# Performance work log

Hardware: AMD Instinct MI355X
Metric: run time of the kernel (lower is better)

## Reference

```python
import jax, jax.numpy as jnp
import numpy as np

NUM_HEADS = 16
HEAD_DIM = 80
DIM = NUM_HEADS * HEAD_DIM
SEQ = 2048
SCALE = HEAD_DIM ** -0.5


def rotate_half(x):
    x1, x2 = jnp.split(x, 2, axis=-1)
    return jnp.concatenate((-x2, x1), axis=-1)


def setup_inputs() -> dict:
    key = jax.random.key(0)
    ks = jax.random.split(key, 8)
    hidden_states = jax.random.normal(ks[0], (SEQ, DIM), dtype=jnp.float32)
    cu_seqlens = jnp.array([0, SEQ], dtype=jnp.int32)  # unused by the math
    # rotary embeddings for head_dim
    inv_freq = 1.0 / (10000.0 ** (jnp.arange(0, HEAD_DIM // 2, dtype=jnp.float32) / (HEAD_DIM // 2)))
    freqs = jnp.outer(jnp.arange(SEQ, dtype=jnp.float32), inv_freq)  # [S, hd/2]
    emb = jnp.concatenate((freqs, freqs), axis=-1)  # [S, hd]
    cos = jnp.cos(emb)
    sin = jnp.sin(emb)
    w_qkv = jax.random.normal(ks[1], (3 * DIM, DIM), dtype=jnp.float32) * (DIM ** -0.5)
    b_qkv = jax.random.normal(ks[2], (3 * DIM,), dtype=jnp.float32) * 0.02
    w_proj = jax.random.normal(ks[3], (DIM, DIM), dtype=jnp.float32) * (DIM ** -0.5)
    b_proj = jax.random.normal(ks[4], (DIM,), dtype=jnp.float32) * 0.02
    return {"hidden_states": hidden_states, "cu_seqlens": cu_seqlens, "cos": cos,
            "sin": sin, "w_qkv": w_qkv, "b_qkv": b_qkv, "w_proj": w_proj, "b_proj": b_proj}


def reference(hidden_states, cu_seqlens, cos, sin, w_qkv, b_qkv, w_proj, b_proj):
    S = hidden_states.shape[0]
    qkv = hidden_states @ w_qkv.T + b_qkv  # [S, 3*D]
    qkv = qkv.reshape(S, 3, NUM_HEADS, HEAD_DIM)
    q, k, v = qkv[:, 0], qkv[:, 1], qkv[:, 2]  # each [S, H, hd]
    c = cos[:, None, :]  # [S, 1, hd]
    s = sin[:, None, :]
    q = q * c + rotate_half(q) * s
    k = k * c + rotate_half(k) * s
    # SDPA, non-causal: [H, S, S]
    scores = jnp.einsum('shd,thd->hst', q, k) * SCALE
    attn = jax.nn.softmax(scores, axis=-1)
    out = jnp.einsum('hst,thd->shd', attn, v).reshape(S, DIM)
    return out @ w_proj.T + b_proj
```

## Files before the change

### kernel.cpp

```cpp
#include <hip/hip_runtime.h>


#define SEQLEN   2048
#define DIMM     1280
#define NHEADS   16
#define HD       80
#define QKV_N    3840
#define NSPLIT   4
#define KVSPAN   (SEQLEN / NSPLIT)
#define QSCALE_LOG2E 0.16130083587064776f

#define KSTRIDE  88
#define VFSTRIDE 24

#define EXP2F(x) __builtin_amdgcn_exp2f(x)

#define GLD16(gptr, lptr)                                                      \
    __builtin_amdgcn_global_load_lds(                                          \
        (const __attribute__((address_space(1))) void*)(gptr),                 \
        (__attribute__((address_space(3))) void*)(lptr), 16, 0, 0)

typedef float f32x4 __attribute__((ext_vector_type(4)));
typedef _Float16 half8 __attribute__((ext_vector_type(8)));
typedef _Float16 half4 __attribute__((ext_vector_type(4)));
typedef _Float16 half2v __attribute__((ext_vector_type(2)));

static __device__ __forceinline__ f32x4 mfma_16x16x32(half8 a, half8 b, f32x4 c) {
    return __builtin_amdgcn_mfma_f32_16x16x32_f16(a, b, c, 0, 0, 0);
}
static __device__ __forceinline__ f32x4 mfma_16x16x16(half4 a, half4 b, f32x4 c) {
    return __builtin_amdgcn_mfma_f32_16x16x16f16(a, b, c, 0, 0, 0);
}
static __device__ __forceinline__ half4 lo4(half8 v) {
    return __builtin_shufflevector(v, v, 0, 1, 2, 3);
}
static __device__ __forceinline__ half4 hi4(half8 v) {
    return __builtin_shufflevector(v, v, 4, 5, 6, 7);
}

__global__ __launch_bounds__(256)
void cast_all(const float* __restrict__ hs, const float* __restrict__ wq,
              const float* __restrict__ wp, _Float16* __restrict__ dhs,
              _Float16* __restrict__ dwq, _Float16* __restrict__ dwp) {
    const int n1 = SEQLEN * DIMM / 4, n2 = QKV_N * DIMM / 4, n3 = DIMM * DIMM / 4;
    int i = blockIdx.x * 256 + threadIdx.x;
    const float4* src; half4* dst; int j;
    if (i < n1)           { src = (const float4*)hs; dst = (half4*)dhs; j = i; }
    else if (i < n1 + n2) { src = (const float4*)wq; dst = (half4*)dwq; j = i - n1; }
    else if (i < n1 + n2 + n3) { src = (const float4*)wp; dst = (half4*)dwp; j = i - n1 - n2; }
    else return;
    const float4 v = src[j];
    half4 h;
    h.x = (_Float16)v.x; h.y = (_Float16)v.y;
    h.z = (_Float16)v.z; h.w = (_Float16)v.w;
    dst[j] = h;
}

template<bool OUT_F16>
__global__ __launch_bounds__(512, 4)
void gemm_bt128(const _Float16* __restrict__ A, const _Float16* __restrict__ B,
                const float* __restrict__ bias, void* __restrict__ Cout,
                int M, int N, int K) {
    __shared__ __align__(16) _Float16 As[2][128 * 32];
    __shared__ __align__(16) _Float16 Bs[2][128 * 32];
    const int tid  = threadIdx.x;
    const int lane = tid & 63;
    const int wave = tid >> 6;
    const int l15  = lane & 15;
    const int quad = lane >> 4;
    const int wm   = wave & 3;
    const int wn   = wave >> 2;
    const long bm = blockIdx.x, bn = blockIdx.y;

    const _Float16* Ag = A + bm * 128 * (long)K;
    const _Float16* Bg = B + bn * 128 * (long)K;

    const int srow = lane >> 2;
    const int scol = (lane & 3) * 8;
    f32x4 acc[2][4] = {};

    for (int k0 = 0; k0 < K; k0 += 64) {
        __syncthreads();
#pragma unroll
        for (int p = 0; p < 2; p++) {
            const int kp = k0 + p * 32;
            const long r = 16 * wave + srow;
            GLD16(Ag + r * K + kp + scol, &As[p][512 * wave + lane * 8]);
            GLD16(Bg + r * K + kp + scol, &Bs[p][512 * wave + lane * 8]);
        }
        __syncthreads();
#pragma unroll
        for (int p = 0; p < 2; p++) {
            half8 af[2], bf[4];
#pragma unroll
            for (int t = 0; t < 2; t++)
                af[t] = *(const half8*)&As[p][(wm * 32 + t * 16 + l15) * 32 + quad * 8];
#pragma unroll
            for (int t = 0; t < 4; t++)
                bf[t] = *(const half8*)&Bs[p][(wn * 64 + t * 16 + l15) * 32 + quad * 8];
#pragma unroll
            for (int mt = 0; mt < 2; mt++)
#pragma unroll
                for (int nt = 0; nt < 4; nt++)
                    acc[mt][nt] = mfma_16x16x32(af[mt], bf[nt], acc[mt][nt]);
        }
    }

    float bv[4];
#pragma unroll
    for (int nt = 0; nt < 4; nt++)
        bv[nt] = bias[bn * 128 + wn * 64 + nt * 16 + l15];

#pragma unroll
    for (int mt = 0; mt < 2; mt++) {
#pragma unroll
        for (int r = 0; r < 4; r++) {
            const long row = bm * 128 + wm * 32 + mt * 16 + quad * 4 + r;
#pragma unroll
            for (int nt = 0; nt < 4; nt++) {
                const long col = bn * 128 + wn * 64 + nt * 16 + l15;
                const float v = acc[mt][nt][r] + bv[nt];
                if (OUT_F16) ((_Float16*)Cout)[row * (long)N + col] = (_Float16)v;
                else         ((float*)Cout)[row * (long)N + col] = v;
            }
        }
    }
}

template<bool OUT_F16>
__global__ __launch_bounds__(256, 2)
void gemm_bt64(const _Float16* __restrict__ A, const _Float16* __restrict__ B,
               const float* __restrict__ bias, void* __restrict__ Cout,
               int M, int N, int K) {
    __shared__ __align__(16) _Float16 As[2][64 * 32];
    __shared__ __align__(16) _Float16 Bs[2][128 * 32];
    const int tid  = threadIdx.x;
    const int lane = tid & 63;
    const int wave = tid >> 6;
    const int l15  = lane & 15;
    const int quad = lane >> 4;
    const int wm   = wave & 1;
    const int wn   = wave >> 1;
    const long bm = blockIdx.x, bn = blockIdx.y;

    const _Float16* Ag = A + bm * 64 * (long)K;
    const _Float16* Bg = B + bn * 128 * (long)K;

    const int srow = lane >> 2;
    const int scol = (lane & 3) * 8;
    f32x4 acc[2][4] = {};

    for (int k0 = 0; k0 < K; k0 += 64) {
        __syncthreads();
#pragma unroll
        for (int p = 0; p < 2; p++) {
            const int kp = k0 + p * 32;
            const long arow = 16 * wave + srow;
            GLD16(Ag + arow * K + kp + scol, &As[p][512 * wave + lane * 8]);
#pragma unroll
            for (int cc = 0; cc < 2; cc++) {
                const int c = wave + cc * 4;
                const long brow = 16 * c + srow;
                GLD16(Bg + brow * K + kp + scol, &Bs[p][512 * c + lane * 8]);
            }
        }
        __syncthreads();
#pragma unroll
        for (int p = 0; p < 2; p++) {
            half8 af[2], bf[4];
#pragma unroll
            for (int t = 0; t < 2; t++)
                af[t] = *(const half8*)&As[p][(wm * 32 + t * 16 + l15) * 32 + quad * 8];
#pragma unroll
            for (int t = 0; t < 4; t++)
                bf[t] = *(const half8*)&Bs[p][(wn * 64 + t * 16 + l15) * 32 + quad * 8];
#pragma unroll
            for (int mt = 0; mt < 2; mt++)
#pragma unroll
                for (int nt = 0; nt < 4; nt++)
                    acc[mt][nt] = mfma_16x16x32(af[mt], bf[nt], acc[mt][nt]);
        }
    }

    float bv[4];
#pragma unroll
    for (int nt = 0; nt < 4; nt++)
        bv[nt] = bias[bn * 128 + wn * 64 + nt * 16 + l15];

#pragma unroll
    for (int mt = 0; mt < 2; mt++) {
#pragma unroll
        for (int r = 0; r < 4; r++) {
            const long row = bm * 64 + wm * 32 + mt * 16 + quad * 4 + r;
#pragma unroll
            for (int nt = 0; nt < 4; nt++) {
                const long col = bn * 128 + wn * 64 + nt * 16 + l15;
                const float v = acc[mt][nt][r] + bv[nt];
                if (OUT_F16) ((_Float16*)Cout)[row * (long)N + col] = (_Float16)v;
                else         ((float*)Cout)[row * (long)N + col] = v;
            }
        }
    }
}

__global__ __launch_bounds__(256)
void rope_repack_t(const _Float16* __restrict__ qkv,
                   const float* __restrict__ cosb,
                   const float* __restrict__ sinb,
                   _Float16* __restrict__ Qh,
                   _Float16* __restrict__ Kh,
                   _Float16* __restrict__ Vt) {
    const int s0 = blockIdx.x * 64;
    const int h  = blockIdx.y;
    __shared__ __align__(16) _Float16 Ts[64 * 88];
    const int tid = threadIdx.x;

    for (int i = tid; i < 640; i += 256) {
        const int r = i / 10, c = (i - r * 10) * 8;
        *(half8*)&Ts[r * 88 + c] =
            *(const half8*)&qkv[(long)(s0 + r) * QKV_N + 2 * DIMM + h * HD + c];
    }

    for (int i = tid; i < 320; i += 256) {
        const int r = i / 5, d = (i - r * 5) * 8;
        const _Float16* row = qkv + (long)(s0 + r) * QKV_N + h * HD;
        const half8 q0 = *(const half8*)&row[d];
        const half8 q1 = *(const half8*)&row[d + 40];
        const half8 k0 = *(const half8*)&row[DIMM + d];
        const half8 k1 = *(const half8*)&row[DIMM + d + 40];
        const float4 cA = *(const float4*)&cosb[(s0 + r) * HD + d];
        const float4 cB = *(const float4*)&cosb[(s0 + r) * HD + d + 4];
        const float4 sA = *(const float4*)&sinb[(s0 + r) * HD + d];
        const float4 sB = *(const float4*)&sinb[(s0 + r) * HD + d + 4];
        half8 qo0, qo1, ko0, ko1;
#pragma unroll
        for (int j = 0; j < 8; j++) {
            const float cj = (j < 4) ? cA[j] : cB[j - 4];
            const float sj = (j < 4) ? sA[j] : sB[j - 4];
            qo0[j] = (_Float16)(((float)q0[j] * cj - (float)q1[j] * sj) * QSCALE_LOG2E);
            qo1[j] = (_Float16)(((float)q1[j] * cj + (float)q0[j] * sj) * QSCALE_LOG2E);
            ko0[j] = (_Float16)((float)k0[j] * cj - (float)k1[j] * sj);
            ko1[j] = (_Float16)((float)k1[j] * cj + (float)k0[j] * sj);
        }
        const long o = ((long)h * SEQLEN + s0 + r) * HD;
        *(half8*)&Qh[o + d]      = qo0;
        *(half8*)&Qh[o + d + 40] = qo1;
        *(half8*)&Kh[o + d]      = ko0;
        *(half8*)&Kh[o + d + 40] = ko1;
    }
    __syncthreads();
    for (int i = tid; i < 640; i += 256) {
        const int d = i >> 3, sc = (i & 7) * 8;
        half8 v;
#pragma unroll
        for (int j = 0; j < 8; j++) v[j] = Ts[(sc + j) * 88 + d];
        *(half8*)&Vt[((long)h * HD + d) * SEQLEN + s0 + sc] = v;
    }
}

__global__ __launch_bounds__(512, 4)
void attn_kernel(const _Float16* __restrict__ Qh, const _Float16* __restrict__ Kh,
                 const _Float16* __restrict__ Vt,
                 _Float16* __restrict__ Ohat0, _Float16* __restrict__ Ohat1,
                 float* __restrict__ Lpart) {
    const int s0 = blockIdx.x * 256;
    const int h  = blockIdx.y;
    const int z  = blockIdx.z;
    __shared__ __align__(16) _Float16 Ks[64 * KSTRIDE];
    __shared__ __align__(16) _Float16 VF[5 * 64 * VFSTRIDE];

    const int tid  = threadIdx.x;
    const int lane = tid & 63;
    const int wave = tid >> 6;
    const int l15  = lane & 15;
    const int quad = lane >> 4;

    const int zBeg = z * KVSPAN, zEnd = zBeg + KVSPAN;

    const _Float16* Qg0 = Qh + ((long)h * SEQLEN + s0 + wave * 32 + l15) * HD;
    const _Float16* Qg1 = Qg0 + 16 * (long)HD;
    const half8 qA0 = *(const half8*)&Qg0[quad * 8];
    const half8 qA1 = *(const half8*)&Qg0[32 + quad * 8];
    const half4 qA2 = *(const half4*)&Qg0[64 + quad * 4];
    const half8 qB0 = *(const half8*)&Qg1[quad * 8];
    const half8 qB1 = *(const half8*)&Qg1[32 + quad * 8];
    const half4 qB2 = *(const half4*)&Qg1[64 + quad * 4];

    int offA, dsA, offB, dsB0, dsB1 = 0, offC = 0, dsC0 = 0, dsC1 = 0;
    {
        const int rA = tid / 10, cA = (tid - rA * 10) * 8;
        offA = rA * HD + cA;
        dsA  = rA * KSTRIDE + cA;
        if (tid < 128) {
            const int cB = tid + 512;
            const int rB = cB / 10, ccB = (cB - rB * 10) * 8;
            offB = rB * HD + ccB;
            dsB0 = rB * KSTRIDE + ccB;
        } else {
            const int v = tid - 128, d = v >> 3, c8 = (v & 7) * 8;
            offB = d * SEQLEN + c8;
            const int nt = d >> 4, ld = d & 15, ct = c8 >> 4, qb = (c8 & 15) >> 2;
            dsB0 = (nt * 64 + qb * 16 + ld) * VFSTRIDE + ct * 4;
            dsB1 = (nt * 64 + (qb + 1) * 16 + ld) * VFSTRIDE + ct * 4;
        }
        if (tid < 256) {
            const int v = tid + 384, d = v >> 3, c8 = (v & 7) * 8;
            offC = d * SEQLEN + c8;
            const int nt = d >> 4, ld = d & 15, ct = c8 >> 4, qb = (c8 & 15) >> 2;
            dsC0 = (nt * 64 + qb * 16 + ld) * VFSTRIDE + ct * 4;
            dsC1 = (nt * 64 + (qb + 1) * 16 + ld) * VFSTRIDE + ct * 4;
        }
    }
    const _Float16* KzBase = Kh + ((long)h * SEQLEN + zBeg) * HD;
    const _Float16* VzBase = Vt + (long)h * HD * SEQLEN + zBeg;

    f32x4 oaccA[5] = {}, oaccB[5] = {};
    float laA0 = 0.f, laA1 = 0.f, laB0 = 0.f, laB1 = 0.f;
    const half2v ones2 = {(_Float16)1.f, (_Float16)1.f};

    for (int t0 = zBeg; t0 < zEnd; t0 += 64) {
        const _Float16* KzT = KzBase + (long)(t0 - zBeg) * HD;
        const _Float16* VzT = VzBase + (t0 - zBeg);
        const half8 a = *(const half8*)(KzT + offA);
        half8 b;
        if (tid < 128) b = *(const half8*)(KzT + offB);
        else           b = *(const half8*)(VzT + offB);
        half8 cv = {};
        if (tid < 256) cv = *(const half8*)(VzT + offC);

        __syncthreads();
        *(half8*)&Ks[dsA] = a;
        if (tid < 128) { *(half8*)&Ks[dsB0] = b; }
        else {
            *(half4*)&VF[dsB0] = lo4(b);
            *(half4*)&VF[dsB1] = hi4(b);
        }
        if (tid < 256) {
            *(half4*)&VF[dsC0] = lo4(cv);
            *(half4*)&VF[dsC1] = hi4(cv);
        }
        __syncthreads();

        f32x4 saA[4] = {}, saB[4] = {};
        __builtin_amdgcn_s_setprio(1);
#pragma unroll
        for (int ct = 0; ct < 4; ct++) {
            const int kb = (ct * 16 + l15) * KSTRIDE;
            const half8 kf0 = *(const half8*)&Ks[kb + quad * 8];
            const half8 kf1 = *(const half8*)&Ks[kb + 32 + quad * 8];
            const half4 kf2 = *(const half4*)&Ks[kb + 64 + quad * 4];
            saA[ct] = mfma_16x16x32(kf0, qA0, saA[ct]);
            saB[ct] = mfma_16x16x32(kf0, qB0, saB[ct]);
            saA[ct] = mfma_16x16x32(kf1, qA1, saA[ct]);
            saB[ct] = mfma_16x16x32(kf1, qB1, saB[ct]);
            saA[ct] = mfma_16x16x16(kf2, qA2, saA[ct]);
            saB[ct] = mfma_16x16x16(kf2, qB2, saB[ct]);
        }
        __builtin_amdgcn_s_setprio(0);

        half4 pbA[4], pbB[4];
#pragma unroll
        for (int ct = 0; ct < 4; ct++) {
            {
                const float e0 = EXP2F(saA[ct][0]);
                const float e1 = EXP2F(saA[ct][1]);
                const float e2 = EXP2F(saA[ct][2]);
                const float e3 = EXP2F(saA[ct][3]);
                const half2v p01 = __builtin_bit_cast(half2v, __builtin_amdgcn_cvt_pkrtz(e0, e1));
                const half2v p23 = __builtin_bit_cast(half2v, __builtin_amdgcn_cvt_pkrtz(e2, e3));
                laA0 = __builtin_amdgcn_fdot2(p01, ones2, laA0, false);
                laA1 = __builtin_amdgcn_fdot2(p23, ones2, laA1, false);
                pbA[ct] = __builtin_shufflevector(p01, p23, 0, 1, 2, 3);
            }
            {
                const float e0 = EXP2F(saB[ct][0]);
                const float e1 = EXP2F(saB[ct][1]);
                const float e2 = EXP2F(saB[ct][2]);
                const float e3 = EXP2F(saB[ct][3]);
                const half2v p01 = __builtin_bit_cast(half2v, __builtin_amdgcn_cvt_pkrtz(e0, e1));
                const half2v p23 = __builtin_bit_cast(half2v, __builtin_amdgcn_cvt_pkrtz(e2, e3));
                laB0 = __builtin_amdgcn_fdot2(p01, ones2, laB0, false);
                laB1 = __builtin_amdgcn_fdot2(p23, ones2, laB1, false);
                pbB[ct] = __builtin_shufflevector(p01, p23, 0, 1, 2, 3);
            }
        }

        __builtin_amdgcn_s_setprio(1);
#pragma unroll
        for (int nt = 0; nt < 5; nt++) {
            const half8 va = *(const half8*)&VF[(nt * 64 + lane) * VFSTRIDE];
            const half8 vb = *(const half8*)&VF[(nt * 64 + lane) * VFSTRIDE + 8];
            oaccA[nt] = mfma_16x16x16(lo4(va), pbA[0], oaccA[nt]);
            oaccB[nt] = mfma_16x16x16(lo4(va), pbB[0], oaccB[nt]);
            oaccA[nt] = mfma_16x16x16(hi4(va), pbA[1], oaccA[nt]);
            oaccB[nt] = mfma_16x16x16(hi4(va), pbB[1], oaccB[nt]);
            oaccA[nt] = mfma_16x16x16(lo4(vb), pbA[2], oaccA[nt]);
            oaccB[nt] = mfma_16x16x16(lo4(vb), pbB[2], oaccB[nt]);
            oaccA[nt] = mfma_16x16x16(hi4(vb), pbA[3], oaccA[nt]);
            oaccB[nt] = mfma_16x16x16(hi4(vb), pbB[3], oaccB[nt]);
        }
        __builtin_amdgcn_s_setprio(0);
    }

    float lA = laA0 + laA1, lB = laB0 + laB1;
    lA += __shfl_xor(lA, 16); lA += __shfl_xor(lA, 32);
    lB += __shfl_xor(lB, 16); lB += __shfl_xor(lB, 32);
    const float invA = 1.0f / lA, invB = 1.0f / lB;

    _Float16* Oz = (z < 2) ? Ohat0 : Ohat1;
    const long obase = ((long)(z & 1) * NHEADS + h) * SEQLEN;
    const long lbase = ((long)z * NHEADS + h) * SEQLEN;
    const long rowA = s0 + wave * 32 + l15;
    const long rowB = rowA + 16;
#pragma unroll
    for (int nt = 0; nt < 5; nt++) {
        half4 oA, oB;
#pragma unroll
        for (int r = 0; r < 4; r++) {
            oA[r] = (_Float16)(oaccA[nt][r] * invA);
            oB[r] = (_Float16)(oaccB[nt][r] * invB);
        }
        *(half4*)&Oz[(obase + rowA) * HD + nt * 16 + quad * 4] = oA;
        *(half4*)&Oz[(obase + rowB) * HD + nt * 16 + quad * 4] = oB;
    }
    if (quad == 0) {
        Lpart[lbase + rowA] = lA;
        Lpart[lbase + rowB] = lB;
    }
}

__global__ __launch_bounds__(256)
void attn_combine(const _Float16* __restrict__ Ohat0,
                  const _Float16* __restrict__ Ohat1,
                  const float* __restrict__ Lp,
                  _Float16* __restrict__ attnb) {
    const int i = blockIdx.x * 256 + threadIdx.x;
    if (i >= SEQLEN * DIMM / 4) return;
    const int flat = i * 4;
    const int s = flat / DIMM;
    const int rem = flat - s * DIMM;
    const int h = rem / HD;
    const int d = rem - h * HD;
    float l[NSPLIT], lsum = 0.f;
#pragma unroll
    for (int zi = 0; zi < NSPLIT; zi++) {
        l[zi] = Lp[((long)zi * NHEADS + h) * SEQLEN + s];
        lsum += l[zi];
    }
    const float invl = 1.0f / lsum;
    float acc[4] = {0.f, 0.f, 0.f, 0.f};
#pragma unroll
    for (int zi = 0; zi < NSPLIT; zi++) {
        const _Float16* Oz = (zi < 2) ? Ohat0 : Ohat1;
        const long obase = ((long)(zi & 1) * NHEADS + h) * SEQLEN;
        const half4 o = *(const half4*)&Oz[(obase + s) * HD + d];
        const float w = l[zi] * invl;
#pragma unroll
        for (int j = 0; j < 4; j++) acc[j] += (float)o[j] * w;
    }
    half4 o;
#pragma unroll
    for (int j = 0; j < 4; j++) o[j] = (_Float16)acc[j];
    *(half4*)&attnb[(long)s * DIMM + rem] = o;
}

extern "C" void kernel_launch(void* const* d_in, const int* in_sizes, int n_in,
                              void* d_out, int out_size, void* d_ws, size_t ws_size,
                              hipStream_t stream) {
    const float* hs     = (const float*)d_in[0];
    const float* cosb   = (const float*)d_in[2];
    const float* sinb   = (const float*)d_in[3];
    const float* w_qkv  = (const float*)d_in[4];
    const float* b_qkv  = (const float*)d_in[5];
    const float* w_proj = (const float*)d_in[6];
    const float* b_proj = (const float*)d_in[7];
    float* out = (float*)d_out;

    _Float16* hsb    = (_Float16*)d_ws;
    _Float16* wqkvb  = hsb    + (long)SEQLEN * DIMM;
    _Float16* wprojb = wqkvb  + (long)QKV_N * DIMM;
    _Float16* qkv    = wprojb + (long)DIMM * DIMM;
    _Float16* Qh     = qkv    + (long)SEQLEN * QKV_N;
    _Float16* Kh     = Qh     + (long)NHEADS * SEQLEN * HD;
    _Float16* Vtb    = Kh     + (long)NHEADS * SEQLEN * HD;
    _Float16* attnb  = Vtb    + (long)NHEADS * HD * SEQLEN;

    _Float16* Ohat0  = (_Float16*)d_ws;
    float*    LpartB = (float*)(Ohat0 + (long)2 * NHEADS * SEQLEN * HD);
    _Float16* Ohat1  = qkv;

    {
        const int ntot = (SEQLEN * DIMM + QKV_N * DIMM + DIMM * DIMM) / 4;
        cast_all<<<(ntot + 255) / 256, 256, 0, stream>>>(
            hs, w_qkv, w_proj, hsb, wqkvb, wprojb);
    }

    gemm_bt128<true><<<dim3(SEQLEN / 128, QKV_N / 128), 512, 0, stream>>>(
        hsb, wqkvb, b_qkv, qkv, SEQLEN, QKV_N, DIMM);

    rope_repack_t<<<dim3(SEQLEN / 64, NHEADS), 256, 0, stream>>>(
        qkv, cosb, sinb, Qh, Kh, Vtb);

    attn_kernel<<<dim3(SEQLEN / 256, NHEADS, NSPLIT), 512, 0, stream>>>(
        Qh, Kh, Vtb, Ohat0, Ohat1, LpartB);

    attn_combine<<<(SEQLEN * DIMM / 4 + 255) / 256, 256, 0, stream>>>(
        Ohat0, Ohat1, LpartB, attnb);

    gemm_bt64<false><<<dim3(SEQLEN / 64, DIMM / 128), 256, 0, stream>>>(
        attnb, wprojb, b_proj, out, SEQLEN, DIMM, DIMM);
}
```

Measured before the change: 187.6 us.

## Double-buffer K/V tiles in attention LDS, widen combine vectors, raise gemm occupancy

The attention kernel now keeps two LDS buffers for its K and V tiles. It prefetches the next 64-key tile into the alternate buffer after the PV MFMAs, which removes one of the two barriers per iteration and lets global loads overlap with compute. The cost is doubled LDS use, about 44KB per block, which may limit occupancy at 4 blocks per CU. The combine kernel now processes 8 halves per thread instead of 4, since HD=80 is divisible by 8, and the projection GEMM's launch-bounds occupancy hint goes from 2 to 4.

```diff
diff --git a/kernel.cpp b/kernel.cpp
--- a/kernel.cpp
+++ b/kernel.cpp
@@ -12,6 +12,8 @@
 
 #define KSTRIDE  88
 #define VFSTRIDE 24
+#define VFOFF    (64 * KSTRIDE)
+#define BUFH     (64 * KSTRIDE + 5 * 64 * VFSTRIDE)
 
 #define EXP2F(x) __builtin_amdgcn_exp2f(x)
 
@@ -128,7 +130,7 @@
 }
 
 template<bool OUT_F16>
-__global__ __launch_bounds__(256, 2)
+__global__ __launch_bounds__(256, 4)
 void gemm_bt64(const _Float16* __restrict__ A, const _Float16* __restrict__ B,
                const float* __restrict__ bias, void* __restrict__ Cout,
                int M, int N, int K) {
@@ -266,8 +268,7 @@
     const int s0 = blockIdx.x * 256;
     const int h  = blockIdx.y;
     const int z  = blockIdx.z;
-    __shared__ __align__(16) _Float16 Ks[64 * KSTRIDE];
-    __shared__ __align__(16) _Float16 VF[5 * 64 * VFSTRIDE];
+    __shared__ __align__(16) _Float16 Sb[2 * BUFH];
 
     const int tid  = threadIdx.x;
     const int lane = tid & 63;
@@ -300,55 +301,55 @@
             const int v = tid - 128, d = v >> 3, c8 = (v & 7) * 8;
             offB = d * SEQLEN + c8;
             const int nt = d >> 4, ld = d & 15, ct = c8 >> 4, qb = (c8 & 15) >> 2;
-            dsB0 = (nt * 64 + qb * 16 + ld) * VFSTRIDE + ct * 4;
-            dsB1 = (nt * 64 + (qb + 1) * 16 + ld) * VFSTRIDE + ct * 4;
+            dsB0 = VFOFF + (nt * 64 + qb * 16 + ld) * VFSTRIDE + ct * 4;
+            dsB1 = VFOFF + (nt * 64 + (qb + 1) * 16 + ld) * VFSTRIDE + ct * 4;
         }
         if (tid < 256) {
             const int v = tid + 384, d = v >> 3, c8 = (v & 7) * 8;
             offC = d * SEQLEN + c8;
             const int nt = d >> 4, ld = d & 15, ct = c8 >> 4, qb = (c8 & 15) >> 2;
-            dsC0 = (nt * 64 + qb * 16 + ld) * VFSTRIDE + ct * 4;
-            dsC1 = (nt * 64 + (qb + 1) * 16 + ld) * VFSTRIDE + ct * 4;
+            dsC0 = VFOFF + (nt * 64 + qb * 16 + ld) * VFSTRIDE + ct * 4;
+            dsC1 = VFOFF + (nt * 64 + (qb + 1) * 16 + ld) * VFSTRIDE + ct * 4;
         }
     }
     const _Float16* KzBase = Kh + ((long)h * SEQLEN + zBeg) * HD;
     const _Float16* VzBase = Vt + (long)h * HD * SEQLEN + zBeg;
+
+    {
+        const half8 a = *(const half8*)(KzBase + offA);
+        half8 b;
+        if (tid < 128) b = *(const half8*)(KzBase + offB);
+        else           b = *(const half8*)(VzBase + offB);
+        half8 cv = {};
+        if (tid < 256) cv = *(const half8*)(VzBase + offC);
+        *(half8*)&Sb[dsA] = a;
+        if (tid < 128) { *(half8*)&Sb[dsB0] = b; }
+        else {
+            *(half4*)&Sb[dsB0] = lo4(b);
+            *(half4*)&Sb[dsB1] = hi4(b);
+        }
+        if (tid < 256) {
+            *(half4*)&Sb[dsC0] = lo4(cv);
+            *(half4*)&Sb[dsC1] = hi4(cv);
+        }
+    }
 
     f32x4 oaccA[5] = {}, oaccB[5] = {};
     float laA0 = 0.f, laA1 = 0.f, laB0 = 0.f, laB1 = 0.f;
     const half2v ones2 = {(_Float16)1.f, (_Float16)1.f};
+    int cb = 0;
 
     for (int t0 = zBeg; t0 < zEnd; t0 += 64) {
-        const _Float16* KzT = KzBase + (long)(t0 - zBeg) * HD;
-        const _Float16* VzT = VzBase + (t0 - zBeg);
-        const half8 a = *(const half8*)(KzT + offA);
-        half8 b;
-        if (tid < 128) b = *(const half8*)(KzT + offB);
-        else           b = *(const half8*)(VzT + offB);
-        half8 cv = {};
-        if (tid < 256) cv = *(const half8*)(VzT + offC);
-
-        __syncthreads();
-        *(half8*)&Ks[dsA] = a;
-        if (tid < 128) { *(half8*)&Ks[dsB0] = b; }
-        else {
-            *(half4*)&VF[dsB0] = lo4(b);
-            *(half4*)&VF[dsB1] = hi4(b);
-        }
-        if (tid < 256) {
-            *(half4*)&VF[dsC0] = lo4(cv);
-            *(half4*)&VF[dsC1] = hi4(cv);
-        }
         __syncthreads();
 
         f32x4 saA[4] = {}, saB[4] = {};
         __builtin_amdgcn_s_setprio(1);
 #pragma unroll
         for (int ct = 0; ct < 4; ct++) {
-            const int kb = (ct * 16 + l15) * KSTRIDE;
-            const half8 kf0 = *(const half8*)&Ks[kb + quad * 8];
-            const half8 kf1 = *(const half8*)&Ks[kb + 32 + quad * 8];
-            const half4 kf2 = *(const half4*)&Ks[kb + 64 + quad * 4];
+            const int kb = cb + (ct * 16 + l15) * KSTRIDE;
+            const half8 kf0 = *(const half8*)&Sb[kb + quad * 8];
+            const half8 kf1 = *(const half8*)&Sb[kb + 32 + quad * 8];
+            const half4 kf2 = *(const half4*)&Sb[kb + 64 + quad * 4];
             saA[ct] = mfma_16x16x32(kf0, qA0, saA[ct]);
             saB[ct] = mfma_16x16x32(kf0, qB0, saB[ct]);
             saA[ct] = mfma_16x16x32(kf1, qA1, saA[ct]);
@@ -388,8 +389,9 @@
         __builtin_amdgcn_s_setprio(1);
 #pragma unroll
         for (int nt = 0; nt < 5; nt++) {
-            const half8 va = *(const half8*)&VF[(nt * 64 + lane) * VFSTRIDE];
-            const half8 vb = *(const half8*)&VF[(nt * 64 + lane) * VFSTRIDE + 8];
+            const int vb0 = cb + VFOFF + (nt * 64 + lane) * VFSTRIDE;
+            const half8 va = *(const half8*)&Sb[vb0];
+            const half8 vb = *(const half8*)&Sb[vb0 + 8];
             oaccA[nt] = mfma_16x16x16(lo4(va), pbA[0], oaccA[nt]);
             oaccB[nt] = mfma_16x16x16(lo4(va), pbB[0], oaccB[nt]);
             oaccA[nt] = mfma_16x16x16(hi4(va), pbA[1], oaccA[nt]);
@@ -400,6 +402,29 @@
             oaccB[nt] = mfma_16x16x16(hi4(vb), pbB[3], oaccB[nt]);
         }
         __builtin_amdgcn_s_setprio(0);
+
+        if (t0 + 64 < zEnd) {
+            const int nb = cb ^ BUFH;
+            const _Float16* KzT = KzBase + (long)(t0 + 64 - zBeg) * HD;
+            const _Float16* VzT = VzBase + (t0 + 64 - zBeg);
+            const half8 a = *(const half8*)(KzT + offA);
+            half8 b;
+            if (tid < 128) b = *(const half8*)(KzT + offB);
+            else           b = *(const half8*)(VzT + offB);
+            half8 cv = {};
+            if (tid < 256) cv = *(const half8*)(VzT + offC);
+            *(half8*)&Sb[nb + dsA] = a;
+            if (tid < 128) { *(half8*)&Sb[nb + dsB0] = b; }
+            else {
+                *(half4*)&Sb[nb + dsB0] = lo4(b);
+                *(half4*)&Sb[nb + dsB1] = hi4(b);
+            }
+            if (tid < 256) {
+                *(half4*)&Sb[nb + dsC0] = lo4(cv);
+                *(half4*)&Sb[nb + dsC1] = hi4(cv);
+            }
+        }
+        cb ^= BUFH;
     }
 
     float lA = laA0 + laA1, lB = laB0 + laB1;
@@ -435,8 +460,8 @@
                   const float* __restrict__ Lp,
                   _Float16* __restrict__ attnb) {
     const int i = blockIdx.x * 256 + threadIdx.x;
-    if (i >= SEQLEN * DIMM / 4) return;
-    const int flat = i * 4;
+    if (i >= SEQLEN * DIMM / 8) return;
+    const int flat = i * 8;
     const int s = flat / DIMM;
     const int rem = flat - s * DIMM;
     const int h = rem / HD;
@@ -448,20 +473,20 @@
         lsum += l[zi];
     }
     const float invl = 1.0f / lsum;
-    float acc[4] = {0.f, 0.f, 0.f, 0.f};
+    float acc[8] = {};
 #pragma unroll
     for (int zi = 0; zi < NSPLIT; zi++) {
         const _Float16* Oz = (zi < 2) ? Ohat0 : Ohat1;
         const long obase = ((long)(zi & 1) * NHEADS + h) * SEQLEN;
-        const half4 o = *(const half4*)&Oz[(obase + s) * HD + d];
+        const half8 o = *(const half8*)&Oz[(obase + s) * HD + d];
         const float w = l[zi] * invl;
 #pragma unroll
-        for (int j = 0; j < 4; j++) acc[j] += (float)o[j] * w;
-    }
-    half4 o;
-#pragma unroll
-    for (int j = 0; j < 4; j++) o[j] = (_Float16)acc[j];
-    *(half4*)&attnb[(long)s * DIMM + rem] = o;
+        for (int j = 0; j < 8; j++) acc[j] += (float)o[j] * w;
+    }
+    half8 o;
+#pragma unroll
+    for (int j = 0; j < 8; j++) o[j] = (_Float16)acc[j];
+    *(half8*)&attnb[(long)s * DIMM + rem] = o;
 }
 
 extern "C" void kernel_launch(void* const* d_in, const int* in_sizes, int n_in,
@@ -504,7 +529,7 @@
     attn_kernel<<<dim3(SEQLEN / 256, NHEADS, NSPLIT), 512, 0, stream>>>(
         Qh, Kh, Vtb, Ohat0, Ohat1, LpartB);
 
-    attn_combine<<<(SEQLEN * DIMM / 4 + 255) / 256, 256, 0, stream>>>(
+    attn_combine<<<(SEQLEN * DIMM / 8 + 255) / 256, 256, 0, stream>>>(
         Ohat0, Ohat1, LpartB, attnb);
 
     gemm_bt64<false><<<dim3(SEQLEN / 64, DIMM / 128), 256, 0, stream>>>(
```

Result: no change. 188.7 us (+0.6%).
